# Kernel optimization log

Hardware: AMD Instinct MI355X
Metric: run time of the kernel (lower is better)

Reference implementation:

```python
import jax, jax.numpy as jnp
import numpy as np


def _cross_head_proj(x, sw, qw1, qw2, kw1, kw2, qdd, kdd):
    # x: [B,N,T,S] attention logits/probs; sw: [N,N]
    # qw1/qw2: [B,T,I,N], kw1/kw2: [B,S,I,N] (I=2 dynamic rank), qdd: [B,T,N], kdd: [B,S,N]
    out = x + jnp.einsum('bnts,nm->bmts', x, sw)
    # low-rank dynamic mixing along query positions (sum over i reproduces the range(2) loop)
    qh = jnp.einsum('bnts,btin->bits', x, qw1)          # [B,I,T,S]
    out = out + jnp.einsum('bits,btin->bnts', qh, qw2)
    # low-rank dynamic mixing along key positions
    kh = jnp.einsum('bnts,bsin->bits', x, kw1)          # [B,I,T,S]
    out = out + jnp.einsum('bits,bsin->bnts', kh, kw2)
    # diagonal (per-head) dynamic terms
    out = out + x * jnp.transpose(qdd, (0, 2, 1))[:, :, :, None]   # [B,N,T,1]
    out = out + x * jnp.transpose(kdd, (0, 2, 1))[:, :, None, :]   # [B,N,1,S]
    return out


def setup_inputs() -> dict:
    key = jax.random.key(0)
    ks = jax.random.split(key, 18)
    B, N, T, S, D, I = 1, 32, 1024, 1024, 128, 2
    scale = 0.05  # dynamic weights come out of tanh/RMSnorm in the original; keep them small
    query = jax.random.normal(ks[0], (B, N, T, D), jnp.float32) * (D ** -0.5)
    k_ = jax.random.normal(ks[1], (B, N, S, D), jnp.float32)
    v_ = jax.random.normal(ks[2], (B, N, S, D), jnp.float32)
    neg = jnp.finfo(jnp.float32).min * 0.5  # matches make_causal_mask
    atten_mask = jnp.where(jnp.arange(S)[None, :] <= jnp.arange(T)[:, None], 0.0, neg).astype(jnp.float32)
    def dws(i0):
        return (
            jax.random.normal(ks[i0 + 0], (N, N), jnp.float32) * scale,
            jax.random.normal(ks[i0 + 1], (B, T, I, N), jnp.float32) * scale,
            jax.random.normal(ks[i0 + 2], (B, T, I, N), jnp.float32) * scale,
            jax.random.normal(ks[i0 + 3], (B, S, I, N), jnp.float32) * scale,
            jax.random.normal(ks[i0 + 4], (B, S, I, N), jnp.float32) * scale,
            jax.random.normal(ks[i0 + 5], (B, T, N), jnp.float32) * scale,
            jax.random.normal(ks[i0 + 6], (B, S, N), jnp.float32) * scale,
        )
    sw_pre, qw1_pre, qw2_pre, kw1_pre, kw2_pre, qdd_pre, kdd_pre = dws(3)
    sw_post, qw1_post, qw2_post, kw1_post, kw2_post, qdd_post, kdd_post = dws(10)
    return {
        'query': query, 'key': k_, 'value': v_, 'atten_mask': atten_mask,
        'sw_pre': sw_pre, 'qw1_pre': qw1_pre, 'qw2_pre': qw2_pre, 'kw1_pre': kw1_pre,
        'kw2_pre': kw2_pre, 'qdd_pre': qdd_pre, 'kdd_pre': kdd_pre,
        'sw_post': sw_post, 'qw1_post': qw1_post, 'qw2_post': qw2_post, 'kw1_post': kw1_post,
        'kw2_post': kw2_post, 'qdd_post': qdd_post, 'kdd_post': kdd_post,
    }


def reference(query, key, value, atten_mask,
              sw_pre, qw1_pre, qw2_pre, kw1_pre, kw2_pre, qdd_pre, kdd_pre,
              sw_post, qw1_post, qw2_post, kw1_post, kw2_post, qdd_post, kdd_post):
    # _atten_context: QK^T -> pre cross-head proj -> mask -> softmax -> post cross-head proj -> AV
    logits = jnp.einsum('bntd,bnsd->bnts', query, key)
    logits = _cross_head_proj(logits, sw_pre, qw1_pre, qw2_pre, kw1_pre, kw2_pre, qdd_pre, kdd_pre)
    logits = logits + atten_mask  # [T,S] broadcasts over [B,N,T,S]
    probs = jax.nn.softmax(logits, axis=-1)
    probs = _cross_head_proj(probs, sw_post, qw1_post, qw2_post, kw1_post, kw2_post, qdd_post, kdd_post)
    return jnp.einsum('bnts,bnsd->bntd', probs, value)
```

## Files before the change

kernel.cpp:

```cpp
#include <hip/hip_runtime.h>
#include <hip/hip_bf16.h>
#include <cstdint>
#include <cstddef>

#define T_DIM 1024
#define S_DIM 1024
#define N_HEADS 32
#define D_HEAD 128

typedef __attribute__((ext_vector_type(8))) short short8;
typedef __attribute__((ext_vector_type(4))) float floatx4;

__device__ inline int pack_bf16(float a, float b) {
    __hip_bfloat162 h = __float22bfloat162_rn(make_float2(a, b));
    int r; __builtin_memcpy(&r, &h, 4); return r;
}
__device__ inline ushort f2b(float x) {
    __hip_bfloat16 h = __float2bfloat16(x);
    ushort u; __builtin_memcpy(&u, &h, 2); return u;
}
__device__ inline float b2f(ushort u) {
    unsigned int v = ((unsigned int)u) << 16;
    float f; __builtin_memcpy(&f, &v, 4); return f;
}

__global__ __launch_bounds__(256) void vt_kernel(const float* __restrict__ V,
                                                 ushort* __restrict__ Vt) {
    const int s0 = blockIdx.x * 64;
    const int n  = blockIdx.y;
    __shared__ float lds[128 * 65];

    const int tid = threadIdx.x;
    const float* Vn = V + ((size_t)n * S_DIM + s0) * D_HEAD;

    #pragma unroll
    for (int it = 0; it < 8; ++it) {
        int idx = tid + it * 256;
        int d4 = idx & 31, s = idx >> 5;
        float4 v = *(const float4*)(Vn + (size_t)s * D_HEAD + d4 * 4);
        lds[(d4 * 4 + 0) * 65 + s] = v.x;
        lds[(d4 * 4 + 1) * 65 + s] = v.y;
        lds[(d4 * 4 + 2) * 65 + s] = v.z;
        lds[(d4 * 4 + 3) * 65 + s] = v.w;
    }
    __syncthreads();

    ushort* Vtn = Vt + (size_t)n * D_HEAD * S_DIM;
    #pragma unroll
    for (int it = 0; it < 4; ++it) {
        int idx = tid + it * 256;
        int sg = idx & 7, d = idx >> 3;
        const float* src = &lds[d * 65 + sg * 8];
        int4 o;
        o.x = pack_bf16(src[0], src[1]);
        o.y = pack_bf16(src[2], src[3]);
        o.z = pack_bf16(src[4], src[5]);
        o.w = pack_bf16(src[6], src[7]);
        *(int4*)&Vtn[(size_t)d * S_DIM + s0 + sg * 8] = o;
    }
}

__global__ __launch_bounds__(256, 2) void qk_mfma(const float* __restrict__ Q,
                                                  const float* __restrict__ K,
                                                  ushort* __restrict__ Lb) {
    const int st = blockIdx.x;
    const int tt = blockIdx.y;
    const int n  = blockIdx.z;
    if (st > tt) return;

    __shared__ int Qt[64 * 64];
    __shared__ int Kt[64 * 64];

    const int tid = threadIdx.x;
    const int wv = tid >> 6, ln = tid & 63;
    const int frow = ln & 15, quad = ln >> 4;

    const float* Qn = Q + ((size_t)n * T_DIM + (size_t)tt * 64) * D_HEAD;
    const float* Kn = K + ((size_t)n * S_DIM + (size_t)st * 64) * D_HEAD;

    #pragma unroll
    for (int rep = 0; rep < 8; ++rep) {
        int idx = tid + rep * 256;
        int row = idx >> 5;
        int c4  = (idx & 31) * 4;
        int p   = c4 >> 1;
        int kb  = p >> 4, w = p & 15;
        int swz = 4 * (row & 3);
        float4 q = *(const float4*)(Qn + (size_t)row * D_HEAD + c4);
        int2 qv; qv.x = pack_bf16(q.x, q.y); qv.y = pack_bf16(q.z, q.w);
        *(int2*)&Qt[row * 64 + kb * 16 + (w ^ swz)] = qv;
        float4 k = *(const float4*)(Kn + (size_t)row * D_HEAD + c4);
        int2 kv; kv.x = pack_bf16(k.x, k.y); kv.y = pack_bf16(k.z, k.w);
        *(int2*)&Kt[row * 64 + kb * 16 + (w ^ swz)] = kv;
    }
    __syncthreads();

    const int swz = 4 * (frow & 3);
    floatx4 acc[4] = {};
    #pragma unroll
    for (int kb = 0; kb < 4; ++kb) {
        const short8 af = *(const short8*)&Qt[(wv * 16 + frow) * 64 + kb * 16 + ((quad * 4) ^ swz)];
        #pragma unroll
        for (int si = 0; si < 4; ++si) {
            const short8 bf = *(const short8*)&Kt[(si * 16 + frow) * 64 + kb * 16 + ((quad * 4) ^ swz)];
            acc[si] = __builtin_amdgcn_mfma_f32_16x16x32_bf16(af, bf, acc[si], 0, 0, 0);
        }
    }
    __syncthreads();

    ushort* Ot = (ushort*)Qt;
    #pragma unroll
    for (int si = 0; si < 4; ++si)
        #pragma unroll
        for (int r = 0; r < 4; ++r)
            Ot[(wv * 16 + quad * 4 + r) * 72 + ((si ^ (quad >> 1)) * 16) + frow] = f2b(acc[si][r]);
    __syncthreads();

    #pragma unroll
    for (int it = 0; it < 2; ++it) {
        int idx = tid + it * 256;
        int row = idx >> 3, col = idx & 7;
        int4 v = *(const int4*)&Ot[row * 72 + ((col * 8) ^ (((row >> 3) & 1) * 16))];
        *(int4*)&Lb[((size_t)n * T_DIM + tt * 64 + row) * S_DIM + st * 64 + col * 8] = v;
    }
}

__global__ __launch_bounds__(256) void mat4_kernel(
        const float* __restrict__ sw_pre,  const float* __restrict__ qw1_pre,
        const float* __restrict__ qw2_pre, const float* __restrict__ qdd_pre,
        const float* __restrict__ kw1_pre, const float* __restrict__ kw2_pre,
        const float* __restrict__ kdd_pre,
        const float* __restrict__ sw_post,  const float* __restrict__ qw1_post,
        const float* __restrict__ qw2_post, const float* __restrict__ qdd_post,
        const float* __restrict__ kw1_post, const float* __restrict__ kw2_post,
        const float* __restrict__ kdd_post,
        ushort* __restrict__ mats) {
    const float *sw, *w1, *w2, *dd;
    float idadd;
    switch (blockIdx.y) {
        case 0:  sw = sw_pre;  w1 = qw1_pre;  w2 = qw2_pre;  dd = qdd_pre;  idadd = 1.0f; break;
        case 1:  sw = nullptr; w1 = kw1_pre;  w2 = kw2_pre;  dd = kdd_pre;  idadd = 0.0f; break;
        case 2:  sw = sw_post; w1 = qw1_post; w2 = qw2_post; dd = qdd_post; idadd = 1.0f; break;
        default: sw = nullptr; w1 = kw1_post; w2 = kw2_post; dd = kdd_post; idadd = 0.0f; break;
    }
    ushort* out = mats + (size_t)blockIdx.y * 1024 * 1024;

    const int t = blockIdx.x;
    const int tid = threadIdx.x;
    const int m = tid >> 3;
    const int n0 = (tid & 7) * 4;

    const float w2m0 = w2[t * 64 + m];
    const float w2m1 = w2[t * 64 + 32 + m];
    const float ddm  = dd[t * 32 + m];

    float v[4];
    #pragma unroll
    for (int j = 0; j < 4; ++j) {
        int n = n0 + j;
        float r = w1[t * 64 + n] * w2m0 + w1[t * 64 + 32 + n] * w2m1;
        if (sw) r += sw[n * 32 + m];
        if (n == m) r += idadd + ddm;
        v[j] = r;
    }
    int p0 = pack_bf16(v[0], v[1]);
    int p1 = pack_bf16(v[2], v[3]);
    int2 st = make_int2(p0, p1);
    *(int2*)&out[(size_t)t * 1024 + m * 32 + n0] = st;
}

__global__ __launch_bounds__(256) void rowstat(const ushort* __restrict__ Lb,
                                               float2* __restrict__ stats) {
    const int wv = threadIdx.x >> 6;
    const int ln = threadIdx.x & 63;
    const int r0 = blockIdx.x * 4 + wv;
    const int t  = r0 & (T_DIM - 1);
    const ushort* row = Lb + (size_t)r0 * S_DIM;

    float v[2][8];
    #pragma unroll
    for (int it = 0; it < 2; ++it) {
        const int i0 = it * 512 + ln * 8;
        #pragma unroll
        for (int j = 0; j < 8; ++j) v[it][j] = -INFINITY;
        if (i0 <= t) {
            uint4 raw = *(const uint4*)&row[i0];
            v[it][0] = b2f((ushort)(raw.x & 0xffff)); v[it][1] = b2f((ushort)(raw.x >> 16));
            v[it][2] = b2f((ushort)(raw.y & 0xffff)); v[it][3] = b2f((ushort)(raw.y >> 16));
            v[it][4] = b2f((ushort)(raw.z & 0xffff)); v[it][5] = b2f((ushort)(raw.z >> 16));
            v[it][6] = b2f((ushort)(raw.w & 0xffff)); v[it][7] = b2f((ushort)(raw.w >> 16));
            #pragma unroll
            for (int j = 0; j < 8; ++j)
                if (i0 + j > t) v[it][j] = -INFINITY;
        }
    }

    float m = -INFINITY;
    #pragma unroll
    for (int it = 0; it < 2; ++it)
        #pragma unroll
        for (int j = 0; j < 8; ++j) m = fmaxf(m, v[it][j]);
    #pragma unroll
    for (int off = 32; off > 0; off >>= 1) m = fmaxf(m, __shfl_xor(m, off));

    float ssum = 0.0f;
    #pragma unroll
    for (int it = 0; it < 2; ++it)
        #pragma unroll
        for (int j = 0; j < 8; ++j)
            ssum += (v[it][j] > -1e37f) ? __expf(v[it][j] - m) : 0.0f;
    #pragma unroll
    for (int off = 32; off > 0; off >>= 1) ssum += __shfl_xor(ssum, off);

    if (ln == 0) stats[r0] = make_float2(m, 1.0f / ssum);
}

template<bool SM>
__global__ __launch_bounds__(256, 4) void proj5(ushort* __restrict__ Lb,
                                                const ushort* __restrict__ Cmat,
                                                const ushort* __restrict__ Kmat,
                                                const float2* __restrict__ stats) {
    const int bid = blockIdx.y * 64 + blockIdx.x;
    const int xcd = bid & 7;
    const int idx = bid >> 3;
    const int ty  = ((idx >> 6) << 3) + xcd;
    const int sx  = idx & 63;

    const int s0 = sx * 16;
    const int t0 = ty * 16;
    if (s0 > t0 + 15) return;

    __shared__ __align__(16) ushort Xs[16 * 648];
    __shared__ __align__(16) float  Kp[16 * 260];

    const int tid = threadIdx.x;
    const int wv = tid >> 6, ln = tid & 63;
    const int frow = ln & 15, quad = ln >> 4;

    #pragma unroll
    for (int it = 0; it < 4; ++it) {
        int slot = tid + it * 256;
        int c    = slot & 1;
        int row  = slot >> 1;
        int nn   = row >> 4, tl = row & 15;
        uint4 ld = *(const uint4*)(Lb + ((size_t)nn * T_DIM + t0 + tl) * S_DIM + s0 + c * 8);
        ushort u[8];
        u[0] = (ushort)(ld.x & 0xffff);  u[1] = (ushort)(ld.x >> 16);
        u[2] = (ushort)(ld.y & 0xffff);  u[3] = (ushort)(ld.y >> 16);
        u[4] = (ushort)(ld.z & 0xffff);  u[5] = (ushort)(ld.z >> 16);
        u[6] = (ushort)(ld.w & 0xffff);  u[7] = (ushort)(ld.w >> 16);
        if (SM) {
            const float2 ms = stats[nn * T_DIM + t0 + tl];
            const int tG = t0 + tl, sbase = s0 + c * 8;
            #pragma unroll
            for (int j = 0; j < 8; ++j) {
                float x = (sbase + j <= tG) ? __expf(b2f(u[j]) - ms.x) * ms.y : 0.0f;
                u[j] = f2b(x);
            }
        }
        ushort* xp = &Xs[tl * 648 + (c * 8) * 40 + nn];
        #pragma unroll
        for (int j = 0; j < 8; ++j) xp[j * 40] = u[j];
    }
    __syncthreads();

    #pragma unroll
    for (int mh = 0; mh < 2; ++mh) {
        #pragma unroll
        for (int k = 0; k < 4; ++k) {
            const int sl = wv * 4 + k;
            const short8 af = *(const short8*)(Kmat + (size_t)(s0 + sl) * 1024 + (mh * 16 + frow) * 32 + quad * 8);
            const short8 bf = *(const short8*)&Xs[frow * 648 + sl * 40 + quad * 8];
            floatx4 z = {0.f, 0.f, 0.f, 0.f};
            floatx4 d = __builtin_amdgcn_mfma_f32_16x16x32_bf16(af, bf, z, 0, 0, 0);
            *(floatx4*)&Kp[frow * 260 + sl * 16 + quad * 4] = d;
        }
        __syncthreads();

        #pragma unroll
        for (int i = 0; i < 4; ++i) {
            const int tl = wv * 4 + i;
            const int tg = t0 + tl;
            const short8 bf = *(const short8*)(Cmat + (size_t)tg * 1024 + (mh * 16 + frow) * 32 + quad * 8);
            const short8 af = *(const short8*)&Xs[tl * 648 + frow * 40 + quad * 8];
            floatx4 z = {0.f, 0.f, 0.f, 0.f};
            floatx4 d = __builtin_amdgcn_mfma_f32_16x16x32_bf16(af, bf, z, 0, 0, 0);
            float v[4];
            #pragma unroll
            for (int r = 0; r < 4; ++r) {
                const int sl = quad * 4 + r;
                float val = d[r] + Kp[tl * 260 + sl * 16 + frow];
                v[r] = (s0 + sl > tg) ? 0.0f : val;
            }
            uint2 stv;
            stv.x = (unsigned)pack_bf16(v[0], v[1]);
            stv.y = (unsigned)pack_bf16(v[2], v[3]);
            *(uint2*)&Lb[((size_t)(mh * 16 + frow) * T_DIM + tg) * S_DIM + s0 + quad * 4] = stv;
        }
        __syncthreads();
    }
}

__global__ __launch_bounds__(256, 4) void av3(const ushort* __restrict__ P,
                                              const ushort* __restrict__ Vt,
                                              float* __restrict__ O) {
    const int tid = threadIdx.x;
    const int wv = tid >> 6, ln = tid & 63;
    const int frow = ln & 15, quad = ln >> 4;
    const int n  = blockIdx.x;
    const int tt = 63 - blockIdx.y;
    const int t0 = tt * 16;

    __shared__ ushort red[4][16][136];

    const ushort* Pn  = P  + ((size_t)n * T_DIM + t0) * S_DIM;
    const ushort* Vtn = Vt + (size_t)n * D_HEAD * S_DIM;

    const int nsteps = (t0 + 47) >> 5;
    const int nclean = t0 >> 5;

    floatx4 acc[8] = {};
    for (int sb = wv; sb < nsteps; sb += 4) {
        short8 a = *(const short8*)(Pn + (size_t)frow * S_DIM + sb * 32 + quad * 8);
        if (sb >= nclean) {
            const int tg  = t0 + frow;
            const int sg0 = sb * 32 + quad * 8;
            #pragma unroll
            for (int j = 0; j < 8; ++j)
                if (sg0 + j > tg) a[j] = 0;
        }
        #pragma unroll
        for (int dc = 0; dc < 8; ++dc) {
            const short8 b = *(const short8*)(Vtn + (size_t)(dc * 16 + frow) * S_DIM + sb * 32 + quad * 8);
            acc[dc] = __builtin_amdgcn_mfma_f32_16x16x32_bf16(a, b, acc[dc], 0, 0, 0);
        }
    }

    #pragma unroll
    for (int dc = 0; dc < 8; ++dc)
        #pragma unroll
        for (int r = 0; r < 4; ++r)
            red[wv][quad * 4 + r][dc * 16 + frow] = f2b(acc[dc][r]);
    __syncthreads();

    #pragma unroll
    for (int it = 0; it < 2; ++it) {
        int idx = tid + it * 256;
        int d4 = idx & 31, tr = idx >> 5;
        float4 v;
        v.x = b2f(red[0][tr][d4 * 4 + 0]) + b2f(red[1][tr][d4 * 4 + 0]) + b2f(red[2][tr][d4 * 4 + 0]) + b2f(red[3][tr][d4 * 4 + 0]);
        v.y = b2f(red[0][tr][d4 * 4 + 1]) + b2f(red[1][tr][d4 * 4 + 1]) + b2f(red[2][tr][d4 * 4 + 1]) + b2f(red[3][tr][d4 * 4 + 1]);
        v.z = b2f(red[0][tr][d4 * 4 + 2]) + b2f(red[1][tr][d4 * 4 + 2]) + b2f(red[2][tr][d4 * 4 + 2]) + b2f(red[3][tr][d4 * 4 + 2]);
        v.w = b2f(red[0][tr][d4 * 4 + 3]) + b2f(red[1][tr][d4 * 4 + 3]) + b2f(red[2][tr][d4 * 4 + 3]) + b2f(red[3][tr][d4 * 4 + 3]);
        *(float4*)&O[((size_t)n * T_DIM + t0 + tr) * D_HEAD + d4 * 4] = v;
    }
}

extern "C" void kernel_launch(void* const* d_in, const int* in_sizes, int n_in,
                              void* d_out, int out_size, void* d_ws, size_t ws_size,
                              hipStream_t stream) {
    const float* Q    = (const float*)d_in[0];
    const float* K    = (const float*)d_in[1];
    const float* V    = (const float*)d_in[2];
    const float* sw_pre  = (const float*)d_in[4];
    const float* qw1_pre = (const float*)d_in[5];
    const float* qw2_pre = (const float*)d_in[6];
    const float* kw1_pre = (const float*)d_in[7];
    const float* kw2_pre = (const float*)d_in[8];
    const float* qdd_pre = (const float*)d_in[9];
    const float* kdd_pre = (const float*)d_in[10];
    const float* sw_post  = (const float*)d_in[11];
    const float* qw1_post = (const float*)d_in[12];
    const float* qw2_post = (const float*)d_in[13];
    const float* kw1_post = (const float*)d_in[14];
    const float* kw2_post = (const float*)d_in[15];
    const float* qdd_post = (const float*)d_in[16];
    const float* kdd_post = (const float*)d_in[17];

    ushort* Lb = (ushort*)d_ws;
    ushort* Vt = (ushort*)((char*)d_ws + (size_t)N_HEADS * T_DIM * S_DIM * 2);
    float*  O  = (float*)d_out;

    ushort* mats  = (ushort*)d_out;
    ushort* Cpre  = mats + 0 * 1024 * 1024;
    ushort* Kpre  = mats + 1 * 1024 * 1024;
    ushort* Cpost = mats + 2 * 1024 * 1024;
    ushort* Kpost = mats + 3 * 1024 * 1024;
    float2* stats = (float2*)((char*)d_out + (size_t)8 * 1024 * 1024);

    mat4_kernel<<<dim3(1024, 4), 256, 0, stream>>>(
        sw_pre, qw1_pre, qw2_pre, qdd_pre, kw1_pre, kw2_pre, kdd_pre,
        sw_post, qw1_post, qw2_post, qdd_post, kw1_post, kw2_post, kdd_post, mats);
    vt_kernel<<<dim3(16, 32), 256, 0, stream>>>(V, Vt);

    qk_mfma<<<dim3(16, 16, 32), 256, 0, stream>>>(Q, K, Lb);
    proj5<false><<<dim3(64, 64), 256, 0, stream>>>(Lb, Cpre, Kpre, nullptr);
    rowstat<<<dim3(8192), 256, 0, stream>>>(Lb, stats);
    proj5<true><<<dim3(64, 64), 256, 0, stream>>>(Lb, Cpost, Kpost, stats);
    av3<<<dim3(32, 64), 256, 0, stream>>>(Lb, Vt, O);
}
```

Measured before the change: 262.6 us.

## Pre-convert Q/K to bf16 and remap QK blocks for XCD locality

Adds a separate pass that converts Q and K from fp32 to bf16 once, so the QK kernel loads half the bytes and skips repeated per-tile conversion; previously each Q/K tile was reread and repacked by up to 16 blocks. The QK grid becomes a flat 1D launch whose block index is remapped so that blocks sharing a head and query tile land on the same XCD, improving L2 reuse. The LDS output staging also drops its XOR swizzle. The cost is an extra kernel launch, extra workspace traffic, and possible LDS bank conflicts in the output stage.

```diff
diff --git a/kernel.cpp b/kernel.cpp
--- a/kernel.cpp
+++ b/kernel.cpp
@@ -22,6 +22,23 @@
 __device__ inline float b2f(ushort u) {
     unsigned int v = ((unsigned int)u) << 16;
     float f; __builtin_memcpy(&f, &v, 4); return f;
+}
+
+__global__ __launch_bounds__(256) void tobf16(const float* __restrict__ Q,
+                                              const float* __restrict__ K,
+                                              ushort* __restrict__ Qb,
+                                              ushort* __restrict__ Kb) {
+    const size_t gid = (size_t)blockIdx.x * 256 + threadIdx.x;
+    #pragma unroll
+    for (int j = 0; j < 2; ++j) {
+        size_t i = gid + (size_t)j * 524288;
+        float4 q = ((const float4*)Q)[i];
+        int2 qp; qp.x = pack_bf16(q.x, q.y); qp.y = pack_bf16(q.z, q.w);
+        ((int2*)Qb)[i] = qp;
+        float4 k = ((const float4*)K)[i];
+        int2 kp; kp.x = pack_bf16(k.x, k.y); kp.y = pack_bf16(k.z, k.w);
+        ((int2*)Kb)[i] = kp;
+    }
 }
 
 __global__ __launch_bounds__(256) void vt_kernel(const float* __restrict__ V,
@@ -60,12 +77,16 @@
     }
 }
 
-__global__ __launch_bounds__(256, 2) void qk_mfma(const float* __restrict__ Q,
-                                                  const float* __restrict__ K,
-                                                  ushort* __restrict__ Lb) {
-    const int st = blockIdx.x;
-    const int tt = blockIdx.y;
-    const int n  = blockIdx.z;
+__global__ __launch_bounds__(256, 2) void qk2(const ushort* __restrict__ Qb,
+                                              const ushort* __restrict__ Kb,
+                                              ushort* __restrict__ Lb) {
+    const int bid  = blockIdx.x;
+    const int xcd  = bid & 7;
+    const int i    = bid >> 3;
+    const int st   = i & 15;
+    const int pair = (i >> 4) * 8 + xcd;
+    const int n    = pair >> 4;
+    const int tt   = pair & 15;
     if (st > tt) return;
 
     __shared__ int Qt[64 * 64];
@@ -75,23 +96,23 @@
     const int wv = tid >> 6, ln = tid & 63;
     const int frow = ln & 15, quad = ln >> 4;
 
-    const float* Qn = Q + ((size_t)n * T_DIM + (size_t)tt * 64) * D_HEAD;
-    const float* Kn = K + ((size_t)n * S_DIM + (size_t)st * 64) * D_HEAD;
+    const ushort* Qn = Qb + ((size_t)n * T_DIM + (size_t)tt * 64) * D_HEAD;
+    const ushort* Kn = Kb + ((size_t)n * S_DIM + (size_t)st * 64) * D_HEAD;
 
     #pragma unroll
     for (int rep = 0; rep < 8; ++rep) {
-        int idx = tid + rep * 256;
-        int row = idx >> 5;
-        int c4  = (idx & 31) * 4;
-        int p   = c4 >> 1;
-        int kb  = p >> 4, w = p & 15;
-        int swz = 4 * (row & 3);
-        float4 q = *(const float4*)(Qn + (size_t)row * D_HEAD + c4);
-        int2 qv; qv.x = pack_bf16(q.x, q.y); qv.y = pack_bf16(q.z, q.w);
-        *(int2*)&Qt[row * 64 + kb * 16 + (w ^ swz)] = qv;
-        float4 k = *(const float4*)(Kn + (size_t)row * D_HEAD + c4);
-        int2 kv; kv.x = pack_bf16(k.x, k.y); kv.y = pack_bf16(k.z, k.w);
-        *(int2*)&Kt[row * 64 + kb * 16 + (w ^ swz)] = kv;
+        int idx = (tid + rep * 256) & 1023;
+        int row = idx >> 4;
+        int c   = idx & 15;
+        int kb  = c >> 2, qw = c & 3;
+        int dst = row * 64 + kb * 16 + ((qw * 4) ^ (4 * (row & 3)));
+        if (rep < 4) {
+            uint4 v = *(const uint4*)(Qn + (size_t)row * D_HEAD + c * 8);
+            *(uint4*)&Qt[dst] = v;
+        } else {
+            uint4 v = *(const uint4*)(Kn + (size_t)row * D_HEAD + c * 8);
+            *(uint4*)&Kt[dst] = v;
+        }
     }
     __syncthreads();
 
@@ -113,14 +134,14 @@
     for (int si = 0; si < 4; ++si)
         #pragma unroll
         for (int r = 0; r < 4; ++r)
-            Ot[(wv * 16 + quad * 4 + r) * 72 + ((si ^ (quad >> 1)) * 16) + frow] = f2b(acc[si][r]);
+            Ot[(wv * 16 + quad * 4 + r) * 72 + si * 16 + frow] = f2b(acc[si][r]);
     __syncthreads();
 
     #pragma unroll
     for (int it = 0; it < 2; ++it) {
         int idx = tid + it * 256;
         int row = idx >> 3, col = idx & 7;
-        int4 v = *(const int4*)&Ot[row * 72 + ((col * 8) ^ (((row >> 3) & 1) * 16))];
+        int4 v = *(const int4*)&Ot[row * 72 + col * 8];
         *(int4*)&Lb[((size_t)n * T_DIM + tt * 64 + row) * S_DIM + st * 64 + col * 8] = v;
     }
 }
@@ -378,7 +399,9 @@
     const float* kdd_post = (const float*)d_in[17];
 
     ushort* Lb = (ushort*)d_ws;
-    ushort* Vt = (ushort*)((char*)d_ws + (size_t)N_HEADS * T_DIM * S_DIM * 2);
+    ushort* Vt = (ushort*)((char*)d_ws + (size_t)64 * 1024 * 1024);
+    ushort* Qb = (ushort*)((char*)d_ws + (size_t)72 * 1024 * 1024);
+    ushort* Kb = (ushort*)((char*)d_ws + (size_t)80 * 1024 * 1024);
     float*  O  = (float*)d_out;
 
     ushort* mats  = (ushort*)d_out;
@@ -391,9 +414,10 @@
     mat4_kernel<<<dim3(1024, 4), 256, 0, stream>>>(
         sw_pre, qw1_pre, qw2_pre, qdd_pre, kw1_pre, kw2_pre, kdd_pre,
         sw_post, qw1_post, qw2_post, qdd_post, kw1_post, kw2_post, kdd_post, mats);
+    tobf16<<<dim3(2048), 256, 0, stream>>>(Q, K, Qb, Kb);
     vt_kernel<<<dim3(16, 32), 256, 0, stream>>>(V, Vt);
 
-    qk_mfma<<<dim3(16, 16, 32), 256, 0, stream>>>(Q, K, Lb);
+    qk2<<<dim3(8192), 256, 0, stream>>>(Qb, Kb, Lb);
     proj5<false><<<dim3(64, 64), 256, 0, stream>>>(Lb, Cpre, Kpre, nullptr);
     rowstat<<<dim3(8192), 256, 0, stream>>>(Lb, stats);
     proj5<true><<<dim3(64, 64), 256, 0, stream>>>(Lb, Cpost, Kpost, stats);
```

New measurement: 259.7 us. About the same (-1.1%).
